# Performance work log

Hardware: AMD Instinct MI355X
Metric: run time of the kernel (lower is better)

## Reference

```python
import jax, jax.numpy as jnp
import numpy as np

B, T, N, FIN, FOUT, EDGE_DIM = 8, 16, 256, 32, 32, 16


def setup_inputs() -> dict:
    key = jax.random.key(0)
    ks = jax.random.split(key, 8)
    def xavier(k, shape):
        fan_in, fan_out = shape[0], shape[1]
        limit = float(np.sqrt(6.0 / (fan_in + fan_out)))
        return jax.random.uniform(k, shape, jnp.float32, -limit, limit)
    return {
        "x": jax.random.normal(ks[0], (B, T, N, FIN), jnp.float32),
        "adj": jax.random.uniform(ks[1], (N, N), jnp.float32),
        # edge_net: Linear(1, edge_dim) -> GELU -> Linear(edge_dim, Fin*Fout)
        "w1": xavier(ks[2], (1, EDGE_DIM)),
        "b1": jnp.zeros((EDGE_DIM,), jnp.float32),
        "w2": xavier(ks[3], (EDGE_DIM, FIN * FOUT)),
        "b2": jnp.zeros((FIN * FOUT,), jnp.float32),
        # node_lin: Linear(Fin, Fout)
        "node_w": xavier(ks[4], (FIN, FOUT)),
        "node_b": jnp.zeros((FOUT,), jnp.float32),
    }


def reference(x, adj, w1, b1, w2, b2, node_w, node_b):
    # edge-conditioned weights: (N, N, Fin, Fout)
    h = jax.nn.gelu(adj[:, :, None] * w1[0] + b1, approximate=False)  # (N,N,E)
    edge_w = (h @ w2 + b2).reshape(N, N, FIN, FOUT)
    # msg[b,t,i,j,:] = sum_f x[b,t,j,f] * edge_w[i,j,f,:]; agg = sum_j msg
    agg = jnp.einsum("btjf,ijfo->btio", x, edge_w)  # (B,T,N,Fout)
    y = jax.nn.gelu(x @ node_w + node_b + agg, approximate=False)
    return y
```

## Files before the change

kernel.cpp:

```cpp
#include <hip/hip_runtime.h>
#include <math.h>

#define NB    256
#define EDIM  16
#define FINN  32
#define FOUTN 32
#define BT    128
#define KKD   4096

typedef __attribute__((ext_vector_type(8))) short short8;
typedef __attribute__((ext_vector_type(4))) float floatx4;

#define MFMA16(a,b,c) __builtin_amdgcn_mfma_f32_16x16x32_bf16((a),(b),(c),0,0,0)

#define BARRIER() asm volatile("s_waitcnt lgkmcnt(0)\n\ts_barrier" ::: "memory")

__device__ __forceinline__ float gelu_f(float v) {
    return 0.5f * v * (1.0f + erff(v * 0.70710678118654752f));
}
__device__ __forceinline__ ushort f2bf(float x) {
    union { float f; unsigned u; } v; v.f = x;
    unsigned r = (v.u + 0x7FFFu + ((v.u >> 16) & 1u)) >> 16;
    return (ushort)r;
}
__device__ __forceinline__ float bf2f(ushort b) {
    union { unsigned u; float f; } v; v.u = ((unsigned)b) << 16; return v.f;
}

__global__ __launch_bounds__(256) void h_kernel(const float* __restrict__ adj,
                                                const float* __restrict__ w1,
                                                const float* __restrict__ b1,
                                                const float* __restrict__ w2,
                                                ushort* __restrict__ Hf,
                                                ushort* __restrict__ w2f) {
    int tid = threadIdx.x;
    if (blockIdx.x >= 128) {
        for (int s = 0; s < 2048; s += 256) {
            int slot = s + tid;
            int e = slot >> 7, r = slot & 127;
            int ot = r >> 6, lane = r & 63;
            int m = lane & 15, quad = lane >> 4;
            const float* src = w2 + (size_t)e * 1024 + (quad * 8) * 32 + ot * 16 + m;
            ushort tmp[8];
            #pragma unroll
            for (int i = 0; i < 8; ++i) tmp[i] = f2bf(src[i * 32]);
            *(int4*)(w2f + (size_t)slot * 8) = *(int4*)tmp;
        }
        return;
    }
    __shared__ float adjs[16][264];
    __shared__ float w1s[16], b1s[16];
    int it = blockIdx.x & 15;
    int kq = blockIdx.x >> 4;
    if (tid < 16) { w1s[tid] = w1[tid]; b1s[tid] = b1[tid]; }
    #pragma unroll
    for (int q = 0; q < 4; ++q) {
        int u = q * 256 + tid;
        int row = u >> 6, c4 = u & 63;
        *(float4*)&adjs[row][c4 * 4] =
            ((const float4*)(adj + ((size_t)it * 16 + row) * 256))[c4];
    }
    __syncthreads();
    #pragma unroll
    for (int q = 0; q < 4; ++q) {
        int u = q * 256 + tid;
        int ks = kq * 16 + (u >> 6);
        int lane = u & 63;
        int m = lane & 15, quad = lane >> 4;
        int e = ks >> 3;
        int j0 = (ks & 7) * 32 + quad * 8;
        float w = w1s[e], b = b1s[e];
        ushort tmp[8];
        #pragma unroll
        for (int d = 0; d < 8; ++d)
            tmp[d] = f2bf(gelu_f(adjs[m][j0 + d] * w + b));
        *(int4*)(Hf + (((size_t)it * 128 + ks) * 64 + lane) * 8) = *(int4*)tmp;
    }
}

#define NCH  16
#define BSP  264
#define XBP  40

__global__ __launch_bounds__(256, 2) void fused_kernel(
        const float* __restrict__ x,      const ushort* __restrict__ w2f,
        const float* __restrict__ b2,     const float* __restrict__ node_w,
        const float* __restrict__ node_b, const ushort* __restrict__ Hf,
        float* __restrict__ out) {
    __shared__ ushort xb[NB][XBP];
    __shared__ ushort Bs[2][32][BSP];
    __shared__ ushort nwT[32][XBP];
    __shared__ float  Sp[8][32];
    __shared__ float  Sv[32];
    __shared__ float  bias2[32];

    int bt   = blockIdx.x;
    int iq   = blockIdx.y;
    int tid  = threadIdx.x;
    int wv   = tid >> 6;
    int lane = tid & 63;
    int m    = lane & 15;
    int quad = lane >> 4;
    int it   = iq * 4 + wv;
    int i0g  = it * 16;

    const ushort* Hlane = Hf + (size_t)it * 128 * 512 + lane * 8;
    const ushort* Wlane = w2f + (size_t)lane * 8;

    short8 areg[2][8];
    short8 wreg[2][2];

    #define ALOAD(dst, c)                                                     \
    {                                                                         \
        _Pragma("unroll")                                                     \
        for (int kk = 0; kk < 8; ++kk)                                        \
            dst[kk] = *(const short8*)(Hlane + ((c) * 8 + kk) * 512);         \
    }
    #define WLOADB(dst, e)                                                    \
    {                                                                         \
        dst[0] = *(const short8*)(Wlane + (size_t)(e) * 1024);                \
        dst[1] = *(const short8*)(Wlane + (size_t)(e) * 1024 + 512);          \
    }

    WLOADB(wreg[0], 0);

    const float4* xg = (const float4*)(x + (size_t)bt * NB * FINN);
    #pragma unroll
    for (int itr = 0; itr < 8; ++itr) {
        int idx4 = itr * 256 + tid;
        float4 v = xg[idx4];
        int j = idx4 >> 3, f = (idx4 & 7) * 4;
        uint2 p;
        p.x = (unsigned)f2bf(v.x) | ((unsigned)f2bf(v.y) << 16);
        p.y = (unsigned)f2bf(v.z) | ((unsigned)f2bf(v.w) << 16);
        *(uint2*)&xb[j][f] = p;
    }
    {
        float4 v = ((const float4*)node_w)[tid];
        int f = tid >> 3, o = (tid & 7) * 4;
        nwT[o + 0][f] = f2bf(v.x); nwT[o + 1][f] = f2bf(v.y);
        nwT[o + 2][f] = f2bf(v.z); nwT[o + 3][f] = f2bf(v.w);
    }
    __syncthreads();

    {
        int f = tid & 31, grp = tid >> 5;
        float s = 0.f;
        for (int j = grp * 32; j < grp * 32 + 32; ++j) s += bf2f(xb[j][f]);
        Sp[grp][f] = s;
    }

    short8 afr[4];
    #pragma unroll
    for (int t = 0; t < 4; ++t)
        afr[t] = *(short8*)&xb[(wv * 4 + t) * 16 + m][quad * 8];

    __syncthreads();
    if (tid < 32) {
        float s = 0.f;
        #pragma unroll
        for (int g = 0; g < 8; ++g) s += Sp[g][tid];
        Sv[tid] = s;
    }

    floatx4 acc[2] = {};

    #define PRODUCE(buf, w)                                                   \
    {                                                                         \
        _Pragma("unroll")                                                     \
        for (int t = 0; t < 4; ++t) {                                         \
            floatx4 z = {0.f, 0.f, 0.f, 0.f};                                 \
            floatx4 d0 = MFMA16(afr[t], w[0], z);                             \
            floatx4 d1 = MFMA16(afr[t], w[1], z);                             \
            int col = (wv * 4 + t) * 16 + quad * 4;                           \
            uint2 p0, p1;                                                     \
            p0.x = (unsigned)f2bf(d0[0]) | ((unsigned)f2bf(d0[1]) << 16);     \
            p0.y = (unsigned)f2bf(d0[2]) | ((unsigned)f2bf(d0[3]) << 16);     \
            p1.x = (unsigned)f2bf(d1[0]) | ((unsigned)f2bf(d1[1]) << 16);     \
            p1.y = (unsigned)f2bf(d1[2]) | ((unsigned)f2bf(d1[3]) << 16);     \
            *(uint2*)&Bs[buf][     m][col] = p0;                              \
            *(uint2*)&Bs[buf][16 + m][col] = p1;                              \
        }                                                                     \
    }
    #define GEMMC(buf, ar)                                                    \
    {                                                                         \
        _Pragma("unroll")                                                     \
        for (int kk = 0; kk < 8; ++kk) {                                      \
            short8 b0 = *(short8*)&Bs[buf][     m][kk * 32 + quad * 8];       \
            short8 b1 = *(short8*)&Bs[buf][16 + m][kk * 32 + quad * 8];       \
            acc[0] = MFMA16(ar[kk], b0, acc[0]);                              \
            acc[1] = MFMA16(ar[kk], b1, acc[1]);                              \
        }                                                                     \
    }

    #pragma unroll
    for (int c = 0; c < NCH; ++c) {
        ALOAD(areg[c & 1], c);
        if (c < NCH - 1) WLOADB(wreg[(c + 1) & 1], c + 1);
        PRODUCE(c & 1, wreg[c & 1]);
        if (c > 0) {
            GEMMC((c - 1) & 1, areg[(c - 1) & 1]);
        } else if (tid < 32) {
            float bb = node_b[tid];
            #pragma unroll
            for (int f = 0; f < FINN; ++f) bb += Sv[f] * b2[f * FOUTN + tid];
            bias2[tid] = bb;
        }
        BARRIER();
    }
    GEMMC((NCH - 1) & 1, areg[(NCH - 1) & 1]);

    {
        short8 xa = *(short8*)&xb[i0g + m][quad * 8];
        #pragma unroll
        for (int tn = 0; tn < 2; ++tn) {
            short8 nb = *(short8*)&nwT[tn * 16 + m][quad * 8];
            acc[tn] = MFMA16(xa, nb, acc[tn]);
        }
    }
    #pragma unroll
    for (int tn = 0; tn < 2; ++tn) {
        int o = tn * 16 + m;
        float bz = bias2[o];
        #pragma unroll
        for (int r = 0; r < 4; ++r) {
            int row = i0g + quad * 4 + r;
            out[((size_t)bt * NB + row) * FOUTN + o] = gelu_f(acc[tn][r] + bz);
        }
    }
}

extern "C" void kernel_launch(void* const* d_in, const int* in_sizes, int n_in,
                              void* d_out, int out_size, void* d_ws, size_t ws_size,
                              hipStream_t stream) {
    const float* x      = (const float*)d_in[0];
    const float* adj    = (const float*)d_in[1];
    const float* w1     = (const float*)d_in[2];
    const float* b1     = (const float*)d_in[3];
    const float* w2     = (const float*)d_in[4];
    const float* b2     = (const float*)d_in[5];
    const float* node_w = (const float*)d_in[6];
    const float* node_b = (const float*)d_in[7];
    float* out = (float*)d_out;

    ushort* Hf  = (ushort*)d_ws;
    ushort* w2f = Hf + (size_t)NB * KKD;

    hipLaunchKernelGGL(h_kernel, dim3(129), dim3(256), 0, stream,
                       adj, w1, b1, w2, Hf, w2f);
    hipLaunchKernelGGL(fused_kernel, dim3(BT, 4), dim3(256), 0, stream,
                       x, w2f, b2, node_w, node_b, Hf, out);
}
```

Before: 95.39 us.

## Process two batch-time slices per block to reuse H and W2 loads

Each block now handles two (b,t) slices instead of one, so the Hf A-fragments and w2f weight fragments loaded from global memory are shared across both slices. This halves the grid to 256 blocks and doubles the LDS buffers and accumulators. Launch bounds drop to one block per CU, which trades occupancy and latency hiding for less redundant global traffic.

```diff
diff --git a/kernel.cpp b/kernel.cpp
--- a/kernel.cpp
+++ b/kernel.cpp
@@ -82,19 +82,19 @@
 #define BSP  264
 #define XBP  40
 
-__global__ __launch_bounds__(256, 2) void fused_kernel(
+__global__ __launch_bounds__(256, 1) void fused_kernel(
         const float* __restrict__ x,      const ushort* __restrict__ w2f,
         const float* __restrict__ b2,     const float* __restrict__ node_w,
         const float* __restrict__ node_b, const ushort* __restrict__ Hf,
         float* __restrict__ out) {
-    __shared__ ushort xb[NB][XBP];
-    __shared__ ushort Bs[2][32][BSP];
+    __shared__ ushort xb[2][NB][XBP];
+    __shared__ ushort Bs[2][2][32][BSP];
     __shared__ ushort nwT[32][XBP];
-    __shared__ float  Sp[8][32];
-    __shared__ float  Sv[32];
-    __shared__ float  bias2[32];
-
-    int bt   = blockIdx.x;
+    __shared__ float  Sp[2][8][32];
+    __shared__ float  Sv[2][32];
+    __shared__ float  bias2[2][32];
+
+    int pr   = blockIdx.x;
     int iq   = blockIdx.y;
     int tid  = threadIdx.x;
     int wv   = tid >> 6;
@@ -103,6 +103,7 @@
     int quad = lane >> 4;
     int it   = iq * 4 + wv;
     int i0g  = it * 16;
+    int bt0  = pr * 2;
 
     const ushort* Hlane = Hf + (size_t)it * 128 * 512 + lane * 8;
     const ushort* Wlane = w2f + (size_t)lane * 8;
@@ -124,16 +125,18 @@
 
     WLOADB(wreg[0], 0);
 
-    const float4* xg = (const float4*)(x + (size_t)bt * NB * FINN);
-    #pragma unroll
-    for (int itr = 0; itr < 8; ++itr) {
+    const float4* xg = (const float4*)(x + (size_t)bt0 * NB * FINN);
+    #pragma unroll
+    for (int itr = 0; itr < 16; ++itr) {
         int idx4 = itr * 256 + tid;
         float4 v = xg[idx4];
-        int j = idx4 >> 3, f = (idx4 & 7) * 4;
+        int b = idx4 >> 11;
+        int w = idx4 & 2047;
+        int j = w >> 3, f = (w & 7) * 4;
         uint2 p;
         p.x = (unsigned)f2bf(v.x) | ((unsigned)f2bf(v.y) << 16);
         p.y = (unsigned)f2bf(v.z) | ((unsigned)f2bf(v.w) << 16);
-        *(uint2*)&xb[j][f] = p;
+        *(uint2*)&xb[b][j][f] = p;
     }
     {
         float4 v = ((const float4*)node_w)[tid];
@@ -145,51 +148,64 @@
 
     {
         int f = tid & 31, grp = tid >> 5;
+        float s0 = 0.f, s1 = 0.f;
+        for (int j = grp * 32; j < grp * 32 + 32; ++j) {
+            s0 += bf2f(xb[0][j][f]);
+            s1 += bf2f(xb[1][j][f]);
+        }
+        Sp[0][grp][f] = s0;
+        Sp[1][grp][f] = s1;
+    }
+
+    short8 afr[2][4];
+    #pragma unroll
+    for (int t = 0; t < 4; ++t) {
+        afr[0][t] = *(short8*)&xb[0][(wv * 4 + t) * 16 + m][quad * 8];
+        afr[1][t] = *(short8*)&xb[1][(wv * 4 + t) * 16 + m][quad * 8];
+    }
+
+    __syncthreads();
+    if (tid < 64) {
+        int b = tid >> 5, f = tid & 31;
         float s = 0.f;
-        for (int j = grp * 32; j < grp * 32 + 32; ++j) s += bf2f(xb[j][f]);
-        Sp[grp][f] = s;
-    }
-
-    short8 afr[4];
-    #pragma unroll
-    for (int t = 0; t < 4; ++t)
-        afr[t] = *(short8*)&xb[(wv * 4 + t) * 16 + m][quad * 8];
-
-    __syncthreads();
-    if (tid < 32) {
-        float s = 0.f;
-        #pragma unroll
-        for (int g = 0; g < 8; ++g) s += Sp[g][tid];
-        Sv[tid] = s;
-    }
-
-    floatx4 acc[2] = {};
+        #pragma unroll
+        for (int g = 0; g < 8; ++g) s += Sp[b][g][f];
+        Sv[b][f] = s;
+    }
+
+    floatx4 acc[2][2] = {};
 
     #define PRODUCE(buf, w)                                                   \
     {                                                                         \
         _Pragma("unroll")                                                     \
-        for (int t = 0; t < 4; ++t) {                                         \
-            floatx4 z = {0.f, 0.f, 0.f, 0.f};                                 \
-            floatx4 d0 = MFMA16(afr[t], w[0], z);                             \
-            floatx4 d1 = MFMA16(afr[t], w[1], z);                             \
-            int col = (wv * 4 + t) * 16 + quad * 4;                           \
-            uint2 p0, p1;                                                     \
-            p0.x = (unsigned)f2bf(d0[0]) | ((unsigned)f2bf(d0[1]) << 16);     \
-            p0.y = (unsigned)f2bf(d0[2]) | ((unsigned)f2bf(d0[3]) << 16);     \
-            p1.x = (unsigned)f2bf(d1[0]) | ((unsigned)f2bf(d1[1]) << 16);     \
-            p1.y = (unsigned)f2bf(d1[2]) | ((unsigned)f2bf(d1[3]) << 16);     \
-            *(uint2*)&Bs[buf][     m][col] = p0;                              \
-            *(uint2*)&Bs[buf][16 + m][col] = p1;                              \
+        for (int b = 0; b < 2; ++b) {                                         \
+            _Pragma("unroll")                                                 \
+            for (int t = 0; t < 4; ++t) {                                     \
+                floatx4 z = {0.f, 0.f, 0.f, 0.f};                             \
+                floatx4 d0 = MFMA16(afr[b][t], w[0], z);                      \
+                floatx4 d1 = MFMA16(afr[b][t], w[1], z);                      \
+                int col = (wv * 4 + t) * 16 + quad * 4;                       \
+                uint2 p0, p1;                                                 \
+                p0.x = (unsigned)f2bf(d0[0]) | ((unsigned)f2bf(d0[1]) << 16); \
+                p0.y = (unsigned)f2bf(d0[2]) | ((unsigned)f2bf(d0[3]) << 16); \
+                p1.x = (unsigned)f2bf(d1[0]) | ((unsigned)f2bf(d1[1]) << 16); \
+                p1.y = (unsigned)f2bf(d1[2]) | ((unsigned)f2bf(d1[3]) << 16); \
+                *(uint2*)&Bs[b][buf][     m][col] = p0;                       \
+                *(uint2*)&Bs[b][buf][16 + m][col] = p1;                       \
+            }                                                                 \
         }                                                                     \
     }
     #define GEMMC(buf, ar)                                                    \
     {                                                                         \
         _Pragma("unroll")                                                     \
         for (int kk = 0; kk < 8; ++kk) {                                      \
-            short8 b0 = *(short8*)&Bs[buf][     m][kk * 32 + quad * 8];       \
-            short8 b1 = *(short8*)&Bs[buf][16 + m][kk * 32 + quad * 8];       \
-            acc[0] = MFMA16(ar[kk], b0, acc[0]);                              \
-            acc[1] = MFMA16(ar[kk], b1, acc[1]);                              \
+            _Pragma("unroll")                                                 \
+            for (int b = 0; b < 2; ++b) {                                     \
+                short8 b0 = *(short8*)&Bs[b][buf][     m][kk * 32 + quad * 8];\
+                short8 b1 = *(short8*)&Bs[b][buf][16 + m][kk * 32 + quad * 8];\
+                acc[b][0] = MFMA16(ar[kk], b0, acc[b][0]);                    \
+                acc[b][1] = MFMA16(ar[kk], b1, acc[b][1]);                    \
+            }                                                                 \
         }                                                                     \
     }
 
@@ -200,32 +216,35 @@
         PRODUCE(c & 1, wreg[c & 1]);
         if (c > 0) {
             GEMMC((c - 1) & 1, areg[(c - 1) & 1]);
-        } else if (tid < 32) {
-            float bb = node_b[tid];
+        } else if (tid < 64) {
+            int b = tid >> 5, o = tid & 31;
+            float bb = node_b[o];
             #pragma unroll
-            for (int f = 0; f < FINN; ++f) bb += Sv[f] * b2[f * FOUTN + tid];
-            bias2[tid] = bb;
+            for (int f = 0; f < FINN; ++f) bb += Sv[b][f] * b2[f * FOUTN + o];
+            bias2[b][o] = bb;
         }
         BARRIER();
     }
     GEMMC((NCH - 1) & 1, areg[(NCH - 1) & 1]);
 
-    {
-        short8 xa = *(short8*)&xb[i0g + m][quad * 8];
+    #pragma unroll
+    for (int b = 0; b < 2; ++b) {
+        short8 xa = *(short8*)&xb[b][i0g + m][quad * 8];
         #pragma unroll
         for (int tn = 0; tn < 2; ++tn) {
             short8 nb = *(short8*)&nwT[tn * 16 + m][quad * 8];
-            acc[tn] = MFMA16(xa, nb, acc[tn]);
-        }
-    }
-    #pragma unroll
-    for (int tn = 0; tn < 2; ++tn) {
-        int o = tn * 16 + m;
-        float bz = bias2[o];
-        #pragma unroll
-        for (int r = 0; r < 4; ++r) {
-            int row = i0g + quad * 4 + r;
-            out[((size_t)bt * NB + row) * FOUTN + o] = gelu_f(acc[tn][r] + bz);
+            acc[b][tn] = MFMA16(xa, nb, acc[b][tn]);
+        }
+        #pragma unroll
+        for (int tn = 0; tn < 2; ++tn) {
+            int o = tn * 16 + m;
+            float bz = bias2[b][o];
+            #pragma unroll
+            for (int r = 0; r < 4; ++r) {
+                int row = i0g + quad * 4 + r;
+                out[((size_t)(bt0 + b) * NB + row) * FOUTN + o] =
+                    gelu_f(acc[b][tn][r] + bz);
+            }
         }
     }
 }
@@ -248,6 +267,6 @@
 
     hipLaunchKernelGGL(h_kernel, dim3(129), dim3(256), 0, stream,
                        adj, w1, b1, w2, Hf, w2f);
-    hipLaunchKernelGGL(fused_kernel, dim3(BT, 4), dim3(256), 0, stream,
+    hipLaunchKernelGGL(fused_kernel, dim3(BT / 2, 4), dim3(256), 0, stream,
                        x, w2f, b2, node_w, node_b, Hf, out);
 }
```

Measured after the change: 101.4 us. +6.3%, slower.
